# Kernel tuning notes

Measured on AMD Instinct MI355X. Metric: run time of the kernel, lower is better.

Reference implementation:

```python
import jax, jax.numpy as jnp
import numpy as np

B, D, L, T, K = 16, 256, 256, 1000, 3
DW, DC = 4, 2  # dim_w, dim_c
CH = 8         # ConvSwishBlock out channels (10 = 1 start + 1 end + 8)


def swish(x):
    return x * jax.nn.sigmoid(x)


def setup_inputs() -> dict:
    key = jax.random.key(0)
    ks = jax.random.split(key, 12)
    # durations ~ U[1,6] per phone -> sum ~ 3.5*L ~ 896 <= T
    durations = 1.0 + 5.0 * jax.random.uniform(ks[0], (B, L), dtype=jnp.float32)
    phoneme = jax.random.normal(ks[1], (B, D, L), dtype=jnp.float32)
    # True = padded phone position
    phone_len = L - (jnp.arange(B) % 4) * 16
    phoneme_mask = (jnp.arange(L)[None, :] >= phone_len[:, None])[:, None, :]
    durations = jnp.where(phoneme_mask[:, 0, :], 0.0, durations)
    s = 0.02
    p = {
        'proj_w_W': s * jax.random.normal(ks[2], (D, D)), 'proj_w_b': jnp.zeros((D,)),
        'conv_w_W': s * jax.random.normal(ks[3], (CH, D, K)), 'conv_w_b': jnp.zeros((CH,)),
        'mlp_w_W': s * jax.random.normal(ks[4], (2 + CH, DW)), 'mlp_w_b': jnp.zeros((DW,)),
        'lin_w_W': s * jax.random.normal(ks[5], (D * DW, D)), 'lin_w_b': jnp.zeros((D,)),
        'proj_c_W': s * jax.random.normal(ks[6], (D, D)), 'proj_c_b': jnp.zeros((D,)),
        'conv_c_W': s * jax.random.normal(ks[7], (CH, D, K)), 'conv_c_b': jnp.zeros((CH,)),
        'mlp_c_W': s * jax.random.normal(ks[8], (2 + CH, DC)), 'mlp_c_b': jnp.zeros((DC,)),
        'lin_c_W': s * jax.random.normal(ks[9], (DW * DC, D)), 'lin_c_b': jnp.zeros((D,)),
    }
    return {'durations': durations, 'phoneme': phoneme, 'phoneme_mask': phoneme_mask, **p}


def _conv_branch(x, phone_pad, projW, projb, convW, convb):
    # x: (B, D, L). 1x1 conv projection, then K-wide 'same' conv to CH channels, swish, mask.
    x = jnp.einsum('od,bdl->bol', projW, x) + projb[None, :, None]
    h = jax.lax.conv_general_dilated(x, convW, (1,), 'SAME',
                                     dimension_numbers=('NCH', 'OIH', 'NCH'))
    h = swish(h + convb[None, :, None])
    h = jnp.where(phone_pad[:, None, :], 0.0, h)
    return h.transpose(0, 2, 1)  # (B, L, CH)


def _forward(durations, phoneme, phoneme_mask,
             proj_w_W, proj_w_b, conv_w_W, conv_w_b, mlp_w_W, mlp_w_b, lin_w_W, lin_w_b,
             proj_c_W, proj_c_b, conv_c_W, conv_c_b, mlp_c_W, mlp_c_b, lin_c_W, lin_c_b):
    phone_pad = phoneme_mask[:, 0, :]                       # (B, L) True = pad
    frame_len = jnp.clip(jnp.round(jnp.sum(durations, -1)), 0, T).astype(jnp.int32)
    frame_pad = jnp.arange(T)[None, :] >= frame_len[:, None]  # (B, T) True = pad
    attn_pad = frame_pad[:, :, None] | phone_pad[:, None, :]  # (B, T, L)

    sd = jnp.cumsum(durations, -1)                          # (B, L) cumulative end times
    sk = sd - durations                                     # (B, L) start times
    t = jnp.arange(1, T + 1, dtype=durations.dtype)
    S = jnp.where(attn_pad, 0.0, t[None, :, None] - sk[:, None, :])                    # (B,T,L)
    E = jnp.where(attn_pad, 0.0, jnp.broadcast_to(sd[:, None, :], attn_pad.shape)
                  - sk[:, None, :])                                                    # (B,T,L)

    # W branch: per-(frame, phone) attention weights over phones
    h_w = _conv_branch(phoneme, phone_pad, proj_w_W, proj_w_b, conv_w_W, conv_w_b)     # (B,L,CH)
    feat_w = jnp.concatenate(
        [S[..., None], E[..., None], jnp.broadcast_to(h_w[:, None], (B, T, L, CH))], -1)
    w = swish(feat_w @ mlp_w_W + mlp_w_b)                   # (B, T, L, DW)
    w = jnp.where(phone_pad[:, None, :, None], -jnp.inf, w)
    w = jax.nn.softmax(w, axis=2)                           # softmax over phones
    w = jnp.where(frame_pad[:, :, None, None], 0.0, w)

    # C branch: auxiliary per-(frame, phone) context
    h_c = _conv_branch(phoneme, phone_pad, proj_c_W, proj_c_b, conv_c_W, conv_c_b)
    feat_c = jnp.concatenate(
        [S[..., None], E[..., None], jnp.broadcast_to(h_c[:, None], (B, T, L, CH))], -1)
    c = swish(feat_c @ mlp_c_W + mlp_c_b)                   # (B, T, L, DC)

    # combine: wh = einsum over phones with phoneme features, wc with c matrix
    wh = jnp.einsum('btnq,bnh->btqh', w, phoneme.transpose(0, 2, 1))  # (B,T,DW,D)
    wh = wh.reshape(B, T, DW * D) @ lin_w_W + lin_w_b                 # (B,T,D)
    wc = jnp.einsum('btnq,btnp->btqp', w, c)                          # (B,T,DW,DC)
    wc = wc.reshape(B, T, DW * DC) @ lin_c_W + lin_c_b                # (B,T,D)
    return wh + wc


def reference(durations, phoneme, phoneme_mask,
              proj_w_W, proj_w_b, conv_w_W, conv_w_b, mlp_w_W, mlp_w_b, lin_w_W, lin_w_b,
              proj_c_W, proj_c_b, conv_c_W, conv_c_b, mlp_c_W, mlp_c_b, lin_c_W, lin_c_b):
    return _forward(durations, phoneme, phoneme_mask,
                    proj_w_W, proj_w_b, conv_w_W, conv_w_b, mlp_w_W, mlp_w_b, lin_w_W, lin_w_b,
                    proj_c_W, proj_c_b, conv_c_W, conv_c_b, mlp_c_W, mlp_c_b, lin_c_W, lin_c_b)
```

## Files before the change

kernel.cpp:

```cpp
#include <hip/hip_runtime.h>


typedef short v8s __attribute__((ext_vector_type(8)));
typedef _Float16 v8h __attribute__((ext_vector_type(8)));
typedef float f4 __attribute__((ext_vector_type(4)));

__device__ __forceinline__ float bf2f(unsigned short h) {
  return __uint_as_float(((unsigned int)h) << 16);
}
__device__ __forceinline__ unsigned short f2bf(float f) {
  unsigned int u = __float_as_uint(f);
  u = (u + 0x7FFFu + ((u >> 16) & 1u)) >> 16;
  return (unsigned short)u;
}
__device__ __forceinline__ float swishf(float x) {
  return x * __builtin_amdgcn_rcpf(1.f + __expf(-x));
}

__global__ __launch_bounds__(256) void k_prep(
    const float* __restrict__ dur, const float* __restrict__ ph,
    const float* __restrict__ liWw,
    const float* __restrict__ cvWw, const float* __restrict__ pjWw,
    const float* __restrict__ pjbw,
    const float* __restrict__ cvWc, const float* __restrict__ pjWc,
    const float* __restrict__ pjbc,
    float* __restrict__ sk, int* __restrict__ frame_len,
    unsigned short* __restrict__ Mb, float* __restrict__ bK,
    unsigned short* __restrict__ LWT, unsigned short* __restrict__ phT) {
  __shared__ float sm[32 * 33];
  int blk = blockIdx.x, tid = threadIdx.x;
  if (blk < 16) {
    int b = blk, l = tid;
    float d = dur[b * 256 + l];
    sm[l] = d;
    __syncthreads();
    for (int off = 1; off < 256; off <<= 1) {
      float v = (l >= off) ? sm[l - off] : 0.f;
      __syncthreads();
      sm[l] += v;
      __syncthreads();
    }
    sk[b * 256 + l] = sm[l] - d;
    if (l == 255) {
      int fl = (int)rintf(sm[255]);
      frame_len[b] = min(max(fl, 0), 1000);
    }
  } else if (blk < 64) {
    int x = blk - 16;
    int br = x / 24, ck = x % 24;
    int ch = ck / 3, k = ck % 3;
    const float* convW = br ? cvWc : cvWw;
    const float* projW = br ? pjWc : pjWw;
    const float* projb = br ? pjbc : pjbw;
    int d = tid;
    float a0 = 0.f, a1 = 0.f, a2 = 0.f, a3 = 0.f;
    for (int o = 0; o < 256; o += 4) {
      a0 += convW[ch * 768 + (o + 0) * 3 + k] * projW[(o + 0) * 256 + d];
      a1 += convW[ch * 768 + (o + 1) * 3 + k] * projW[(o + 1) * 256 + d];
      a2 += convW[ch * 768 + (o + 2) * 3 + k] * projW[(o + 2) * 256 + d];
      a3 += convW[ch * 768 + (o + 3) * 3 + k] * projW[(o + 3) * 256 + d];
    }
    Mb[(br * 24 + ck) * 256 + d] = f2bf((a0 + a1) + (a2 + a3));
    if (tid < 64) {
      float pb = 0.f;
      for (int o = tid; o < 256; o += 64)
        pb += convW[ch * 768 + o * 3 + k] * projb[o];
#pragma unroll
      for (int off = 1; off < 64; off <<= 1) pb += __shfl_xor(pb, off);
      if (tid == 0) bK[br * 24 + ck] = pb;
    }
  } else if (blk < 320) {
    int idx = blk - 64;
    int kt = idx & 31, ot = idx >> 5;
    int tx = tid & 31, ty = tid >> 5;
#pragma unroll
    for (int r = 0; r < 4; r++) {
      int row = ty + r * 8;
      sm[row * 33 + tx] = liWw[(size_t)(kt * 32 + row) * 256 + ot * 32 + tx];
    }
    __syncthreads();
#pragma unroll
    for (int r = 0; r < 4; r++) {
      int row = ty + r * 8;
      LWT[(size_t)(ot * 32 + row) * 1024 + kt * 32 + tx] =
          f2bf(sm[tx * 33 + row]);
    }
  } else {
    int idx = blk - 320;
    int ht = idx & 7, lt = (idx >> 3) & 7, b = idx >> 6;
    int tx = tid & 31, ty = tid >> 5;
#pragma unroll
    for (int r = 0; r < 4; r++) {
      int row = ty + r * 8;
      sm[row * 33 + tx] =
          ph[(size_t)b * 65536 + (size_t)(ht * 32 + row) * 256 + lt * 32 + tx];
    }
    __syncthreads();
#pragma unroll
    for (int r = 0; r < 4; r++) {
      int row = ty + r * 8;
      phT[(size_t)b * 65536 + (size_t)(lt * 32 + row) * 256 + ht * 32 + tx] =
          f2bf(sm[tx * 33 + row]);
    }
  }
}

__global__ __launch_bounds__(256) void k_convG(
    const unsigned short* __restrict__ phT, const unsigned short* __restrict__ Mb,
    const float* __restrict__ bK, const float* __restrict__ cvbw,
    const float* __restrict__ cvbc, const float* __restrict__ dur,
    const float* __restrict__ sk, const float* __restrict__ mlpWw,
    const float* __restrict__ mlpbw, const float* __restrict__ mlpWc,
    const float* __restrict__ mlpbc, const unsigned short* __restrict__ LWT,
    float* __restrict__ Lbw, float* __restrict__ Laux,
    float* __restrict__ maxAb, _Float16* __restrict__ G) {
  __shared__ __align__(16) float C[256 * 49];
  __shared__ float redm[4][4];
  int blk = blockIdx.x;
  int tid = threadIdx.x, wave = tid >> 6, lane = tid & 63;
  int quad = lane >> 4, col = lane & 15;
  if (blk < 16) {
    int b = blk;
    int l0 = wave * 64;
    const unsigned short* Ab = phT + (size_t)b * 65536;
    f4 acc[4][3] = {};
#pragma unroll
    for (int k0 = 0; k0 < 256; k0 += 32) {
      v8s af[4], bf[3];
#pragma unroll
      for (int lt = 0; lt < 4; lt++)
        af[lt] = *(const v8s*)(Ab + (size_t)(l0 + lt * 16 + col) * 256 + k0 + quad * 8);
#pragma unroll
      for (int ct = 0; ct < 3; ct++)
        bf[ct] = *(const v8s*)(Mb + (size_t)(ct * 16 + col) * 256 + k0 + quad * 8);
#pragma unroll
      for (int lt = 0; lt < 4; lt++)
#pragma unroll
        for (int ct = 0; ct < 3; ct++)
          acc[lt][ct] = __builtin_amdgcn_mfma_f32_16x16x32_bf16(af[lt], bf[ct],
                                                                acc[lt][ct], 0, 0, 0);
    }
#pragma unroll
    for (int lt = 0; lt < 4; lt++)
#pragma unroll
      for (int ct = 0; ct < 3; ct++)
#pragma unroll
        for (int r = 0; r < 4; r++)
          C[(l0 + lt * 16 + quad * 4 + r) * 49 + ct * 16 + col] = acc[lt][ct][r];
    __syncthreads();
    int l = tid;
    float dv = dur[b * 256 + l];
    bool vld = (dv != 0.f);
    float hv[2][8];
#pragma unroll
    for (int br = 0; br < 2; br++) {
      const float* convb = br ? cvbc : cvbw;
#pragma unroll
      for (int ch = 0; ch < 8; ch++) {
        int ck = br * 24 + ch * 3;
        float v = convb[ch] + bK[ck + 1] + C[l * 49 + ck + 1];
        if (l > 0) v += bK[ck + 0] + C[(l - 1) * 49 + ck + 0];
        if (l < 255) v += bK[ck + 2] + C[(l + 1) * 49 + ck + 2];
        hv[br][ch] = vld ? swishf(v) : 0.f;
      }
    }
    float skl = sk[b * 256 + l];
    float A[4];
#pragma unroll
    for (int q = 0; q < 4; q++) {
      float a = mlpbw[q] + dv * mlpWw[4 + q] - skl * mlpWw[q];
#pragma unroll
      for (int ch = 0; ch < 8; ch++) a += hv[0][ch] * mlpWw[(2 + ch) * 4 + q];
      A[q] = vld ? a : -1e30f;
    }
    float bb0 = mlpbc[0] + dv * mlpWc[2] - skl * mlpWc[0];
    float bb1 = mlpbc[1] + dv * mlpWc[3] - skl * mlpWc[1];
#pragma unroll
    for (int ch = 0; ch < 8; ch++) {
      bb0 += hv[1][ch] * mlpWc[(2 + ch) * 2 + 0];
      bb1 += hv[1][ch] * mlpWc[(2 + ch) * 2 + 1];
    }
    float4 Av = {A[0], A[1], A[2], A[3]};
    ((float4*)Lbw)[b * 256 + l] = Av;
    float4 Xv = {bb0, bb1, vld ? 1.f : 0.f, 0.f};
    ((float4*)Laux)[b * 256 + l] = Xv;
    float m0 = A[0], m1 = A[1], m2 = A[2], m3 = A[3];
#pragma unroll
    for (int off = 1; off < 64; off <<= 1) {
      m0 = fmaxf(m0, __shfl_xor(m0, off));
      m1 = fmaxf(m1, __shfl_xor(m1, off));
      m2 = fmaxf(m2, __shfl_xor(m2, off));
      m3 = fmaxf(m3, __shfl_xor(m3, off));
    }
    if (lane == 0) {
      redm[wave][0] = m0;
      redm[wave][1] = m1;
      redm[wave][2] = m2;
      redm[wave][3] = m3;
    }
    __syncthreads();
    if (tid < 4)
      maxAb[b * 4 + tid] = fmaxf(fmaxf(redm[0][tid], redm[1][tid]),
                                 fmaxf(redm[2][tid], redm[3][tid]));
  } else {
    int idx = blk - 16;
    int b = (idx & 7) * 2 + ((idx >> 3) & 1);
    int sub = idx >> 4;
    int q = sub >> 3, rem = sub & 7;
    int mo = (rem >> 2) * 128, nl = (rem & 3) * 64;
    int wm = (wave & 1) * 64, wn = (wave >> 1) * 32;
    const unsigned short* Ag = LWT + (size_t)q * 256;
    const unsigned short* Bg = phT + (size_t)b * 65536;
    size_t aoff[4], boff[2];
#pragma unroll
    for (int mt = 0; mt < 4; mt++)
      aoff[mt] = (size_t)(mo + wm + mt * 16 + col) * 1024 + quad * 8;
#pragma unroll
    for (int nt = 0; nt < 2; nt++)
      boff[nt] = (size_t)(nl + wn + nt * 16 + col) * 256 + quad * 8;

    v8s ra[2][4], rb[2][2];
#pragma unroll
    for (int c = 0; c < 2; c++) {
#pragma unroll
      for (int mt = 0; mt < 4; mt++)
        ra[c][mt] = *(const v8s*)(Ag + aoff[mt] + c * 32);
#pragma unroll
      for (int nt = 0; nt < 2; nt++)
        rb[c][nt] = *(const v8s*)(Bg + boff[nt] + c * 32);
    }
    f4 acc[4][2] = {};
#pragma unroll
    for (int s = 0; s < 8; s++) {
#pragma unroll
      for (int mt = 0; mt < 4; mt++)
#pragma unroll
        for (int nt = 0; nt < 2; nt++)
          acc[mt][nt] = __builtin_amdgcn_mfma_f32_16x16x32_bf16(
              ra[s & 1][mt], rb[s & 1][nt], acc[mt][nt], 0, 0, 0);
      if (s < 6) {
#pragma unroll
        for (int mt = 0; mt < 4; mt++)
          ra[s & 1][mt] = *(const v8s*)(Ag + aoff[mt] + (s + 2) * 32);
#pragma unroll
        for (int nt = 0; nt < 2; nt++)
          rb[s & 1][nt] = *(const v8s*)(Bg + boff[nt] + (s + 2) * 32);
      }
    }
    _Float16* Gb = G + (size_t)b * 262144 + q * 256;
#pragma unroll
    for (int mt = 0; mt < 4; mt++)
#pragma unroll
      for (int r = 0; r < 4; r++) {
        int orow = mo + wm + mt * 16 + quad * 4 + r;
#pragma unroll
        for (int nt = 0; nt < 2; nt++) {
          int lcol = nl + wn + nt * 16 + col;
          Gb[(size_t)orow * 1024 + lcol] = (_Float16)acc[mt][nt][r];
        }
      }
  }
}

__global__ __launch_bounds__(1024, 4) void k_fuse(
    const float* __restrict__ Lbw, const float* __restrict__ Laux,
    const float* __restrict__ maxAb, const int* __restrict__ frame_len,
    const float* __restrict__ mlpWw, const float* __restrict__ mlpWc,
    const _Float16* __restrict__ G, const float* __restrict__ lwb,
    const float* __restrict__ lcb, const float* __restrict__ LC,
    float* __restrict__ out) {
  __shared__ __align__(16) _Float16 Asm[64 * 512];
  __shared__ __align__(16) float4 Lb4[272];
  __shared__ __align__(16) float4 Lx4[272];
  __shared__ float bias_s[256];
  __shared__ float lcs[8][256];
  __shared__ float wcs[64][8];

  int idx = blockIdx.x;
  int b = (idx & 7) * 2 + ((idx >> 3) & 1);
  int t0 = (idx >> 4) * 64;
  int tid = threadIdx.x, wave = tid >> 6, lane = tid & 63;
  int quad = lane >> 4, col = lane & 15;

  int fl = frame_len[b];
  if (t0 >= fl) {
    int o = tid & 255;
    float v = lwb[o] + lcb[o];
    for (int r = tid >> 8; r < 64; r += 4) {
      int t = t0 + r;
      if (t < 1000) out[((size_t)(b * 1000 + t)) * 256 + o] = v;
    }
    return;
  }

  if (tid < 256) {
    float4 av = ((const float4*)Lbw)[b * 256 + tid];
    float4 xv = ((const float4*)Laux)[b * 256 + tid];
    int li = tid + (tid >> 4);
    Lb4[li] = av;
    Lx4[li] = xv;
    bias_s[tid] = lwb[tid] + lcb[tid];
  }
  for (int i = tid; i < 2048; i += 1024) lcs[i >> 8][i & 255] = LC[i];

  float4 mx4 = ((const float4*)maxAb)[b];
  float mw0 = mlpWw[0], mw1 = mlpWw[1], mw2 = mlpWw[2], mw3 = mlpWw[3];
  float mc0 = mlpWc[0], mc1 = mlpWc[1];

  int l_grp = lane & 15;
  int row = wave * 4 + (lane >> 4);
  int t = t0 + row;
  bool live = (t < fl);
  float tp1 = (float)(t + 1);
  int rsw = row & 7;
  int asw = col & 7;
  int wn = wave * 16;
  f4 acc[4] = {};

  const _Float16* GA =
      G + (size_t)b * 262144 + (size_t)(wn + col) * 1024 + quad * 8;

  __syncthreads();

#pragma unroll
  for (int p = 0; p < 2; ++p) {
    const _Float16* Gp = GA + p * 512;
    v8h rb[4];
#pragma unroll
    for (int c = 0; c < 4; ++c) rb[c] = *(const v8h*)(Gp + c * 32);

    float mq0 = p ? mw2 : mw0;
    float mq1 = p ? mw3 : mw1;
    float mxa = p ? mx4.z : mx4.x;
    float mxb = p ? mx4.w : mx4.y;
    float m0 = live ? fmaxf(mxa + tp1 * mq0, 0.f) : 1e30f;
    float m1 = live ? fmaxf(mxb + tp1 * mq1, 0.f) : 1e30f;
    float s0 = 0.f, s1 = 0.f, p00 = 0.f, p01 = 0.f, p10 = 0.f, p11 = 0.f;
    v8h e0[2], e1[2];
#pragma unroll
    for (int j = 0; j < 16; ++j) {
      int l = l_grp * 16 + j;
      int li = l + (l >> 4);
      float4 A4 = Lb4[li];
      float4 ax = Lx4[li];
      float cp0 = swishf(ax.x + tp1 * mc0);
      float cp1 = swishf(ax.y + tp1 * mc1);
      float Aq0 = p ? A4.z : A4.x;
      float Aq1 = p ? A4.w : A4.y;
      _Float16 eh0 = (_Float16)(__expf(swishf(Aq0 + tp1 * mq0) - m0) * ax.z);
      _Float16 eh1 = (_Float16)(__expf(swishf(Aq1 + tp1 * mq1) - m1) * ax.z);
      e0[j >> 3][j & 7] = eh0;
      e1[j >> 3][j & 7] = eh1;
      float f0 = (float)eh0, f1 = (float)eh1;
      s0 += f0;
      s1 += f1;
      p00 += f0 * cp0;
      p01 += f0 * cp1;
      p10 += f1 * cp0;
      p11 += f1 * cp1;
    }
#pragma unroll
    for (int off = 1; off < 16; off <<= 1) {
      s0 += __shfl_xor(s0, off);
      s1 += __shfl_xor(s1, off);
      p00 += __shfl_xor(p00, off);
      p01 += __shfl_xor(p01, off);
      p10 += __shfl_xor(p10, off);
      p11 += __shfl_xor(p11, off);
    }
    float iv0 = live ? 1.0f / s0 : 0.f;
    float iv1 = live ? 1.0f / s1 : 0.f;

    if (p) __syncthreads();

    if (l_grp == 0) {
      wcs[row][p * 4 + 0] = p00 * iv0;
      wcs[row][p * 4 + 1] = p01 * iv0;
      wcs[row][p * 4 + 2] = p10 * iv1;
      wcs[row][p * 4 + 3] = p11 * iv1;
    }
#pragma unroll
    for (int c = 0; c < 2; ++c) {
      int sl = (l_grp * 2 + c) ^ rsw;
      v8h w0, w1;
#pragma unroll
      for (int k = 0; k < 8; ++k) {
        w0[k] = (_Float16)((float)e0[c][k] * iv0);
        w1[k] = (_Float16)((float)e1[c][k] * iv1);
      }
      *(v8h*)&Asm[(row * 64 + sl) * 8] = w0;
      *(v8h*)&Asm[(row * 64 + 32 + sl) * 8] = w1;
    }
    __syncthreads();
    __builtin_amdgcn_s_setprio(1);
#pragma unroll
    for (int s = 0; s < 16; ++s) {
      int slk = s * 4 + quad;
      v8h af[4];
#pragma unroll
      for (int mt = 0; mt < 4; ++mt)
        af[mt] = *(const v8h*)&Asm[((mt * 16 + col) * 64 + (slk ^ asw)) * 8];
#pragma unroll
      for (int mt = 0; mt < 4; ++mt)
        acc[mt] = __builtin_amdgcn_mfma_f32_16x16x32_f16(af[mt], rb[s & 3],
                                                         acc[mt], 0, 0, 0);
      if (s < 12) rb[s & 3] = *(const v8h*)(Gp + (s + 4) * 32);
    }
    __builtin_amdgcn_s_setprio(0);
  }
#pragma unroll
  for (int mt = 0; mt < 4; ++mt)
#pragma unroll
    for (int r = 0; r < 4; ++r) {
      int lrow = mt * 16 + quad * 4 + r;
      int trow = t0 + lrow;
      if (trow < 1000) {
        float4 wa = *(const float4*)&wcs[lrow][0];
        float4 wb = *(const float4*)&wcs[lrow][4];
        float wcl[8] = {wa.x, wa.y, wa.z, wa.w, wb.x, wb.y, wb.z, wb.w};
        int oc = wn + col;
        float v = acc[mt][r] + bias_s[oc];
#pragma unroll
        for (int jj = 0; jj < 8; ++jj) v = fmaf(wcl[jj], lcs[jj][oc], v);
        out[((size_t)(b * 1000 + trow)) * 256 + oc] = v;
      }
    }
}

extern "C" void kernel_launch(void* const* d_in, const int* in_sizes, int n_in,
                              void* d_out, int out_size, void* d_ws, size_t ws_size,
                              hipStream_t stream) {
  const float* dur  = (const float*)d_in[0];
  const float* ph   = (const float*)d_in[1];
  const float* pjWw = (const float*)d_in[3];
  const float* pjbw = (const float*)d_in[4];
  const float* cvWw = (const float*)d_in[5];
  const float* cvbw = (const float*)d_in[6];
  const float* mlWw = (const float*)d_in[7];
  const float* mlbw = (const float*)d_in[8];
  const float* liWw = (const float*)d_in[9];
  const float* libw = (const float*)d_in[10];
  const float* pjWc = (const float*)d_in[11];
  const float* pjbc = (const float*)d_in[12];
  const float* cvWc = (const float*)d_in[13];
  const float* cvbc = (const float*)d_in[14];
  const float* mlWc = (const float*)d_in[15];
  const float* mlbc = (const float*)d_in[16];
  const float* liWc = (const float*)d_in[17];
  const float* libc = (const float*)d_in[18];
  float* out = (float*)d_out;

  float* f = (float*)d_ws;
  size_t o = 0;
  float* sk = f + o;            o += 4096;
  int* fl = (int*)(f + o);      o += 16;
  float* bK = f + o;            o += 64;
  unsigned short* Mb = (unsigned short*)(f + o); o += 6144;
  float* Lbw = f + o;           o += 16384;
  float* Laux = f + o;          o += 16384;
  float* mxA = f + o;           o += 64;
  _Float16* G = (_Float16*)(f + o);              o += 2097152;
  unsigned short* phT = (unsigned short*)(f + o); o += 524288;
  unsigned short* LWT = (unsigned short*)(f + o); o += 131072;

  k_prep<<<1344, 256, 0, stream>>>(dur, ph, liWw, cvWw, pjWw, pjbw, cvWc, pjWc,
                                   pjbc, sk, fl, Mb, bK, LWT, phT);
  k_convG<<<528, 256, 0, stream>>>(phT, Mb, bK, cvbw, cvbc, dur, sk, mlWw,
                                   mlbw, mlWc, mlbc, LWT, Lbw, Laux, mxA, G);
  k_fuse<<<256, 1024, 0, stream>>>(Lbw, Laux, mxA, fl, mlWw, mlWc, G, libw,
                                   libc, liWc, out);
}
```

Before: 173.2 us.

## Overlap second-half softmax weight computation with first-half MFMA loop

Unrolls the two-pass loop by hand and interleaves the exp/swish computation of the second half's attention weights into the first half's MFMA loop, one phone per step. The aim is to hide transcendental ALU work behind matrix-core work instead of running the two serially. This raises register pressure, since the second half's weight and accumulator registers stay live during the MFMA loop, which may reduce occupancy or cause spills.

```diff
diff --git a/kernel.cpp b/kernel.cpp
--- a/kernel.cpp
+++ b/kernel.cpp
@@ -319,22 +319,18 @@
 
   const _Float16* GA =
       G + (size_t)b * 262144 + (size_t)(wn + col) * 1024 + quad * 8;
+  const _Float16* Gp0 = GA;
+  const _Float16* Gp1 = GA + 512;
 
   __syncthreads();
 
-#pragma unroll
-  for (int p = 0; p < 2; ++p) {
-    const _Float16* Gp = GA + p * 512;
-    v8h rb[4];
-#pragma unroll
-    for (int c = 0; c < 4; ++c) rb[c] = *(const v8h*)(Gp + c * 32);
-
-    float mq0 = p ? mw2 : mw0;
-    float mq1 = p ? mw3 : mw1;
-    float mxa = p ? mx4.z : mx4.x;
-    float mxb = p ? mx4.w : mx4.y;
-    float m0 = live ? fmaxf(mxa + tp1 * mq0, 0.f) : 1e30f;
-    float m1 = live ? fmaxf(mxb + tp1 * mq1, 0.f) : 1e30f;
+  v8h rb[4];
+#pragma unroll
+  for (int c = 0; c < 4; ++c) rb[c] = *(const v8h*)(Gp0 + c * 32);
+
+  float m0a = live ? fmaxf(mx4.x + tp1 * mw0, 0.f) : 1e30f;
+  float m1a = live ? fmaxf(mx4.y + tp1 * mw1, 0.f) : 1e30f;
+  {
     float s0 = 0.f, s1 = 0.f, p00 = 0.f, p01 = 0.f, p10 = 0.f, p11 = 0.f;
     v8h e0[2], e1[2];
 #pragma unroll
@@ -345,10 +341,8 @@
       float4 ax = Lx4[li];
       float cp0 = swishf(ax.x + tp1 * mc0);
       float cp1 = swishf(ax.y + tp1 * mc1);
-      float Aq0 = p ? A4.z : A4.x;
-      float Aq1 = p ? A4.w : A4.y;
-      _Float16 eh0 = (_Float16)(__expf(swishf(Aq0 + tp1 * mq0) - m0) * ax.z);
-      _Float16 eh1 = (_Float16)(__expf(swishf(Aq1 + tp1 * mq1) - m1) * ax.z);
+      _Float16 eh0 = (_Float16)(__expf(swishf(A4.x + tp1 * mw0) - m0a) * ax.z);
+      _Float16 eh1 = (_Float16)(__expf(swishf(A4.y + tp1 * mw1) - m1a) * ax.z);
       e0[j >> 3][j & 7] = eh0;
       e1[j >> 3][j & 7] = eh1;
       float f0 = (float)eh0, f1 = (float)eh1;
@@ -370,14 +364,11 @@
     }
     float iv0 = live ? 1.0f / s0 : 0.f;
     float iv1 = live ? 1.0f / s1 : 0.f;
-
-    if (p) __syncthreads();
-
     if (l_grp == 0) {
-      wcs[row][p * 4 + 0] = p00 * iv0;
-      wcs[row][p * 4 + 1] = p01 * iv0;
-      wcs[row][p * 4 + 2] = p10 * iv1;
-      wcs[row][p * 4 + 3] = p11 * iv1;
+      wcs[row][0] = p00 * iv0;
+      wcs[row][1] = p01 * iv0;
+      wcs[row][2] = p10 * iv1;
+      wcs[row][3] = p11 * iv1;
     }
 #pragma unroll
     for (int c = 0; c < 2; ++c) {
@@ -391,23 +382,102 @@
       *(v8h*)&Asm[(row * 64 + sl) * 8] = w0;
       *(v8h*)&Asm[(row * 64 + 32 + sl) * 8] = w1;
     }
-    __syncthreads();
-    __builtin_amdgcn_s_setprio(1);
-#pragma unroll
-    for (int s = 0; s < 16; ++s) {
-      int slk = s * 4 + quad;
-      v8h af[4];
-#pragma unroll
-      for (int mt = 0; mt < 4; ++mt)
-        af[mt] = *(const v8h*)&Asm[((mt * 16 + col) * 64 + (slk ^ asw)) * 8];
-#pragma unroll
-      for (int mt = 0; mt < 4; ++mt)
-        acc[mt] = __builtin_amdgcn_mfma_f32_16x16x32_f16(af[mt], rb[s & 3],
-                                                         acc[mt], 0, 0, 0);
-      if (s < 12) rb[s & 3] = *(const v8h*)(Gp + (s + 4) * 32);
-    }
-    __builtin_amdgcn_s_setprio(0);
-  }
+  }
+  __syncthreads();
+
+  float m0b = live ? fmaxf(mx4.z + tp1 * mw2, 0.f) : 1e30f;
+  float m1b = live ? fmaxf(mx4.w + tp1 * mw3, 0.f) : 1e30f;
+  float s0b = 0.f, s1b = 0.f, p00b = 0.f, p01b = 0.f, p10b = 0.f, p11b = 0.f;
+  v8h e0b[2], e1b[2];
+  __builtin_amdgcn_s_setprio(1);
+#pragma unroll
+  for (int s = 0; s < 16; ++s) {
+    int slk = s * 4 + quad;
+    v8h af[4];
+#pragma unroll
+    for (int mt = 0; mt < 4; ++mt)
+      af[mt] = *(const v8h*)&Asm[((mt * 16 + col) * 64 + (slk ^ asw)) * 8];
+#pragma unroll
+    for (int mt = 0; mt < 4; ++mt)
+      acc[mt] = __builtin_amdgcn_mfma_f32_16x16x32_f16(af[mt], rb[s & 3],
+                                                       acc[mt], 0, 0, 0);
+    if (s < 12) rb[s & 3] = *(const v8h*)(Gp0 + (s + 4) * 32);
+    {
+      int l = l_grp * 16 + s;
+      int li = l + (l >> 4);
+      float4 A4 = Lb4[li];
+      float4 ax = Lx4[li];
+      float cp0 = swishf(ax.x + tp1 * mc0);
+      float cp1 = swishf(ax.y + tp1 * mc1);
+      _Float16 eh0 = (_Float16)(__expf(swishf(A4.z + tp1 * mw2) - m0b) * ax.z);
+      _Float16 eh1 = (_Float16)(__expf(swishf(A4.w + tp1 * mw3) - m1b) * ax.z);
+      e0b[s >> 3][s & 7] = eh0;
+      e1b[s >> 3][s & 7] = eh1;
+      float f0 = (float)eh0, f1 = (float)eh1;
+      s0b += f0;
+      s1b += f1;
+      p00b += f0 * cp0;
+      p01b += f0 * cp1;
+      p10b += f1 * cp0;
+      p11b += f1 * cp1;
+    }
+  }
+  __builtin_amdgcn_s_setprio(0);
+
+  v8h rb1[4];
+#pragma unroll
+  for (int c = 0; c < 4; ++c) rb1[c] = *(const v8h*)(Gp1 + c * 32);
+
+#pragma unroll
+  for (int off = 1; off < 16; off <<= 1) {
+    s0b += __shfl_xor(s0b, off);
+    s1b += __shfl_xor(s1b, off);
+    p00b += __shfl_xor(p00b, off);
+    p01b += __shfl_xor(p01b, off);
+    p10b += __shfl_xor(p10b, off);
+    p11b += __shfl_xor(p11b, off);
+  }
+  float iv0b = live ? 1.0f / s0b : 0.f;
+  float iv1b = live ? 1.0f / s1b : 0.f;
+
+  __syncthreads();
+
+  if (l_grp == 0) {
+    wcs[row][4] = p00b * iv0b;
+    wcs[row][5] = p01b * iv0b;
+    wcs[row][6] = p10b * iv1b;
+    wcs[row][7] = p11b * iv1b;
+  }
+#pragma unroll
+  for (int c = 0; c < 2; ++c) {
+    int sl = (l_grp * 2 + c) ^ rsw;
+    v8h w0, w1;
+#pragma unroll
+    for (int k = 0; k < 8; ++k) {
+      w0[k] = (_Float16)((float)e0b[c][k] * iv0b);
+      w1[k] = (_Float16)((float)e1b[c][k] * iv1b);
+    }
+    *(v8h*)&Asm[(row * 64 + sl) * 8] = w0;
+    *(v8h*)&Asm[(row * 64 + 32 + sl) * 8] = w1;
+  }
+  __syncthreads();
+
+  __builtin_amdgcn_s_setprio(1);
+#pragma unroll
+  for (int s = 0; s < 16; ++s) {
+    int slk = s * 4 + quad;
+    v8h af[4];
+#pragma unroll
+    for (int mt = 0; mt < 4; ++mt)
+      af[mt] = *(const v8h*)&Asm[((mt * 16 + col) * 64 + (slk ^ asw)) * 8];
+#pragma unroll
+    for (int mt = 0; mt < 4; ++mt)
+      acc[mt] = __builtin_amdgcn_mfma_f32_16x16x32_f16(af[mt], rb1[s & 3],
+                                                       acc[mt], 0, 0, 0);
+    if (s < 12) rb1[s & 3] = *(const v8h*)(Gp1 + (s + 4) * 32);
+  }
+  __builtin_amdgcn_s_setprio(0);
+
 #pragma unroll
   for (int mt = 0; mt < 4; ++mt)
 #pragma unroll
```

After: 169.7 us. -2.0%, faster.

## Split fused kernel into producer and consumer waves with double-buffered LDS

Applied to the files above, without the earlier changes.

Splits the 16 waves of k_fuse into 8 producer waves and 8 consumer waves. The producers compute the softmax weights one dw-slice at a time into a double-buffered LDS tile, while the consumers run MFMA over the previous slice against G. Each consumer wave now covers 32 output columns, and G fragments for the next slice are prefetched. The aim is to overlap the exp/swish ALU work with the matrix-core work. In exchange, only half the waves do each job, there are more barriers, and consumer register pressure is higher.

```diff
diff --git a/kernel.cpp b/kernel.cpp
--- a/kernel.cpp
+++ b/kernel.cpp
@@ -269,7 +269,7 @@
     const _Float16* __restrict__ G, const float* __restrict__ lwb,
     const float* __restrict__ lcb, const float* __restrict__ LC,
     float* __restrict__ out) {
-  __shared__ __align__(16) _Float16 Asm[64 * 512];
+  __shared__ __align__(16) _Float16 AsmB[2][64 * 32 * 8];
   __shared__ __align__(16) float4 Lb4[272];
   __shared__ __align__(16) float4 Lx4[272];
   __shared__ float bias_s[256];
@@ -304,127 +304,139 @@
   for (int i = tid; i < 2048; i += 1024) lcs[i >> 8][i & 255] = LC[i];
 
   float4 mx4 = ((const float4*)maxAb)[b];
-  float mw0 = mlpWw[0], mw1 = mlpWw[1], mw2 = mlpWw[2], mw3 = mlpWw[3];
+  float mwA0 = mlpWw[0], mwA1 = mlpWw[1], mwA2 = mlpWw[2], mwA3 = mlpWw[3];
   float mc0 = mlpWc[0], mc1 = mlpWc[1];
 
-  int l_grp = lane & 15;
-  int row = wave * 4 + (lane >> 4);
-  int t = t0 + row;
-  bool live = (t < fl);
-  float tp1 = (float)(t + 1);
-  int rsw = row & 7;
-  int asw = col & 7;
-  int wn = wave * 16;
-  f4 acc[4] = {};
-
+  bool isProd = wave < 8;
+
+  int prow = (wave & 7) * 8 + (lane >> 3);
+  int l_grp8 = lane & 7;
+  int pt = t0 + prow;
+  bool plive = pt < fl;
+  float ptp1 = (float)(pt + 1);
+
+  int wn = (wave & 7) * 32;
   const _Float16* GA =
       G + (size_t)b * 262144 + (size_t)(wn + col) * 1024 + quad * 8;
+  const _Float16* GB = GA + (size_t)16 * 1024;
+  f4 acc[4][2] = {};
+  v8h rb4[4][2];
+
+#define PRODUCE(P, BUF)                                                        \
+  do {                                                                         \
+    float mq = (P == 0) ? mwA0 : (P == 1) ? mwA1 : (P == 2) ? mwA2 : mwA3;     \
+    float mxq = (P == 0) ? mx4.x : (P == 1) ? mx4.y : (P == 2) ? mx4.z : mx4.w;\
+    float m = plive ? fmaxf(mxq + ptp1 * mq, 0.f) : 1e30f;                     \
+    float s0 = 0.f, pw0 = 0.f, pw1 = 0.f;                                      \
+    v8h e[4];                                                                  \
+    _Pragma("unroll") for (int j = 0; j < 32; ++j) {                           \
+      int l = l_grp8 * 32 + j;                                                 \
+      int li = l + (l >> 4);                                                   \
+      float4 A4 = Lb4[li];                                                     \
+      float4 ax = Lx4[li];                                                     \
+      float cp0 = swishf(ax.x + ptp1 * mc0);                                   \
+      float cp1 = swishf(ax.y + ptp1 * mc1);                                   \
+      float Aq = (P == 0) ? A4.x : (P == 1) ? A4.y : (P == 2) ? A4.z : A4.w;   \
+      _Float16 eh = (_Float16)(__expf(swishf(Aq + ptp1 * mq) - m) * ax.z);     \
+      e[j >> 3][j & 7] = eh;                                                   \
+      float f = (float)eh;                                                     \
+      s0 += f;                                                                 \
+      pw0 += f * cp0;                                                          \
+      pw1 += f * cp1;                                                          \
+    }                                                                          \
+    _Pragma("unroll") for (int off = 1; off < 8; off <<= 1) {                  \
+      s0 += __shfl_xor(s0, off);                                               \
+      pw0 += __shfl_xor(pw0, off);                                             \
+      pw1 += __shfl_xor(pw1, off);                                             \
+    }                                                                          \
+    float iv = plive ? 1.0f / s0 : 0.f;                                        \
+    if (l_grp8 == 0) {                                                         \
+      wcs[prow][(P)*2 + 0] = pw0 * iv;                                         \
+      wcs[prow][(P)*2 + 1] = pw1 * iv;                                         \
+    }                                                                          \
+    _Pragma("unroll") for (int cc = 0; cc < 4; ++cc) {                         \
+      v8h w;                                                                   \
+      _Pragma("unroll") for (int k = 0; k < 8; ++k)                            \
+          w[k] = (_Float16)((float)e[cc][k] * iv);                             \
+      int sl = (l_grp8 * 4 + cc) ^ (prow & 7);                                 \
+      *(v8h*)&AsmB[BUF][((prow * 32) + sl) * 8] = w;                           \
+    }                                                                          \
+  } while (0)
+
+#define CONSUME(P, BUF, NP)                                                    \
+  do {                                                                         \
+    const _Float16* gpa = GA + (P)*256;                                        \
+    const _Float16* gpb = GB + (P)*256;                                        \
+    __builtin_amdgcn_s_setprio(1);                                             \
+    _Pragma("unroll") for (int s = 0; s < 8; ++s) {                            \
+      v8h af[4];                                                               \
+      _Pragma("unroll") for (int mt = 0; mt < 4; ++mt)                         \
+          af[mt] = *(const v8h*)&AsmB[BUF][(((mt * 16 + col) * 32) +           \
+                                            ((s * 4 + quad) ^ (col & 7))) *    \
+                                           8];                                 \
+      _Pragma("unroll") for (int mt = 0; mt < 4; ++mt) {                       \
+        acc[mt][0] = __builtin_amdgcn_mfma_f32_16x16x32_f16(                   \
+            af[mt], rb4[s & 3][0], acc[mt][0], 0, 0, 0);                       \
+        acc[mt][1] = __builtin_amdgcn_mfma_f32_16x16x32_f16(                   \
+            af[mt], rb4[s & 3][1], acc[mt][1], 0, 0, 0);                       \
+      }                                                                        \
+      if (s < 4) {                                                             \
+        rb4[s][0] = *(const v8h*)(gpa + (s + 4) * 32);                         \
+        rb4[s][1] = *(const v8h*)(gpb + (s + 4) * 32);                         \
+      } else if ((NP) >= 0) {                                                  \
+        rb4[s - 4][0] = *(const v8h*)(GA + (NP)*256 + (s - 4) * 32);           \
+        rb4[s - 4][1] = *(const v8h*)(GB + (NP)*256 + (s - 4) * 32);           \
+      }                                                                        \
+    }                                                                          \
+    __builtin_amdgcn_s_setprio(0);                                             \
+  } while (0)
 
   __syncthreads();
 
-#pragma unroll
-  for (int p = 0; p < 2; ++p) {
-    const _Float16* Gp = GA + p * 512;
-    v8h rb[4];
-#pragma unroll
-    for (int c = 0; c < 4; ++c) rb[c] = *(const v8h*)(Gp + c * 32);
-
-    float mq0 = p ? mw2 : mw0;
-    float mq1 = p ? mw3 : mw1;
-    float mxa = p ? mx4.z : mx4.x;
-    float mxb = p ? mx4.w : mx4.y;
-    float m0 = live ? fmaxf(mxa + tp1 * mq0, 0.f) : 1e30f;
-    float m1 = live ? fmaxf(mxb + tp1 * mq1, 0.f) : 1e30f;
-    float s0 = 0.f, s1 = 0.f, p00 = 0.f, p01 = 0.f, p10 = 0.f, p11 = 0.f;
-    v8h e0[2], e1[2];
-#pragma unroll
-    for (int j = 0; j < 16; ++j) {
-      int l = l_grp * 16 + j;
-      int li = l + (l >> 4);
-      float4 A4 = Lb4[li];
-      float4 ax = Lx4[li];
-      float cp0 = swishf(ax.x + tp1 * mc0);
-      float cp1 = swishf(ax.y + tp1 * mc1);
-      float Aq0 = p ? A4.z : A4.x;
-      float Aq1 = p ? A4.w : A4.y;
-      _Float16 eh0 = (_Float16)(__expf(swishf(Aq0 + tp1 * mq0) - m0) * ax.z);
-      _Float16 eh1 = (_Float16)(__expf(swishf(Aq1 + tp1 * mq1) - m1) * ax.z);
-      e0[j >> 3][j & 7] = eh0;
-      e1[j >> 3][j & 7] = eh1;
-      float f0 = (float)eh0, f1 = (float)eh1;
-      s0 += f0;
-      s1 += f1;
-      p00 += f0 * cp0;
-      p01 += f0 * cp1;
-      p10 += f1 * cp0;
-      p11 += f1 * cp1;
-    }
-#pragma unroll
-    for (int off = 1; off < 16; off <<= 1) {
-      s0 += __shfl_xor(s0, off);
-      s1 += __shfl_xor(s1, off);
-      p00 += __shfl_xor(p00, off);
-      p01 += __shfl_xor(p01, off);
-      p10 += __shfl_xor(p10, off);
-      p11 += __shfl_xor(p11, off);
-    }
-    float iv0 = live ? 1.0f / s0 : 0.f;
-    float iv1 = live ? 1.0f / s1 : 0.f;
-
-    if (p) __syncthreads();
-
-    if (l_grp == 0) {
-      wcs[row][p * 4 + 0] = p00 * iv0;
-      wcs[row][p * 4 + 1] = p01 * iv0;
-      wcs[row][p * 4 + 2] = p10 * iv1;
-      wcs[row][p * 4 + 3] = p11 * iv1;
-    }
-#pragma unroll
-    for (int c = 0; c < 2; ++c) {
-      int sl = (l_grp * 2 + c) ^ rsw;
-      v8h w0, w1;
-#pragma unroll
-      for (int k = 0; k < 8; ++k) {
-        w0[k] = (_Float16)((float)e0[c][k] * iv0);
-        w1[k] = (_Float16)((float)e1[c][k] * iv1);
+  if (isProd) {
+    PRODUCE(0, 0);
+  } else {
+#pragma unroll
+    for (int c = 0; c < 4; ++c) {
+      rb4[c][0] = *(const v8h*)(GA + c * 32);
+      rb4[c][1] = *(const v8h*)(GB + c * 32);
+    }
+  }
+  __syncthreads();
+  if (isProd) PRODUCE(1, 1);
+  else        CONSUME(0, 0, 1);
+  __syncthreads();
+  if (isProd) PRODUCE(2, 0);
+  else        CONSUME(1, 1, 2);
+  __syncthreads();
+  if (isProd) PRODUCE(3, 1);
+  else        CONSUME(2, 0, 3);
+  __syncthreads();
+  if (!isProd) {
+    CONSUME(3, 1, -1);
+#pragma unroll
+    for (int mt = 0; mt < 4; ++mt)
+#pragma unroll
+      for (int r = 0; r < 4; ++r) {
+        int lrow = mt * 16 + quad * 4 + r;
+        int trow = t0 + lrow;
+        if (trow < 1000) {
+          float4 wa = *(const float4*)&wcs[lrow][0];
+          float4 wb = *(const float4*)&wcs[lrow][4];
+          float wcl[8] = {wa.x, wa.y, wa.z, wa.w, wb.x, wb.y, wb.z, wb.w};
+#pragma unroll
+          for (int nt = 0; nt < 2; ++nt) {
+            int oc = wn + nt * 16 + col;
+            float v = acc[mt][nt][r] + bias_s[oc];
+#pragma unroll
+            for (int jj = 0; jj < 8; ++jj) v = fmaf(wcl[jj], lcs[jj][oc], v);
+            out[((size_t)(b * 1000 + trow)) * 256 + oc] = v;
+          }
+        }
       }
-      *(v8h*)&Asm[(row * 64 + sl) * 8] = w0;
-      *(v8h*)&Asm[(row * 64 + 32 + sl) * 8] = w1;
-    }
-    __syncthreads();
-    __builtin_amdgcn_s_setprio(1);
-#pragma unroll
-    for (int s = 0; s < 16; ++s) {
-      int slk = s * 4 + quad;
-      v8h af[4];
-#pragma unroll
-      for (int mt = 0; mt < 4; ++mt)
-        af[mt] = *(const v8h*)&Asm[((mt * 16 + col) * 64 + (slk ^ asw)) * 8];
-#pragma unroll
-      for (int mt = 0; mt < 4; ++mt)
-        acc[mt] = __builtin_amdgcn_mfma_f32_16x16x32_f16(af[mt], rb[s & 3],
-                                                         acc[mt], 0, 0, 0);
-      if (s < 12) rb[s & 3] = *(const v8h*)(Gp + (s + 4) * 32);
-    }
-    __builtin_amdgcn_s_setprio(0);
-  }
-#pragma unroll
-  for (int mt = 0; mt < 4; ++mt)
-#pragma unroll
-    for (int r = 0; r < 4; ++r) {
-      int lrow = mt * 16 + quad * 4 + r;
-      int trow = t0 + lrow;
-      if (trow < 1000) {
-        float4 wa = *(const float4*)&wcs[lrow][0];
-        float4 wb = *(const float4*)&wcs[lrow][4];
-        float wcl[8] = {wa.x, wa.y, wa.z, wa.w, wb.x, wb.y, wb.z, wb.w};
-        int oc = wn + col;
-        float v = acc[mt][r] + bias_s[oc];
-#pragma unroll
-        for (int jj = 0; jj < 8; ++jj) v = fmaf(wcl[jj], lcs[jj][oc], v);
-        out[((size_t)(b * 1000 + trow)) * 256 + oc] = v;
-      }
-    }
+  }
+#undef PRODUCE
+#undef CONSUME
 }
 
 extern "C" void kernel_launch(void* const* d_in, const int* in_sizes, int n_in,
```

Measured after the change: 188.1 us. 8.6% more time.
